# Optimization experiments

Hardware: AMD Instinct MI355X
Metric: run time of the kernel (lower is better)

Reference implementation:

```python
import jax, jax.numpy as jnp
import numpy as np

N_NODES = 50000
N_EDGES = 800000
N_GRAPHS = 64
IN_DIM = 128
HID = 32
HEADS = 4
EDGE_DIM = 8
OUT = 10


def setup_inputs() -> dict:
    key = jax.random.key(0)
    ks = jax.random.split(key, 20)
    s = 0.1
    inp = {
        "x": jax.random.normal(ks[0], (N_NODES, IN_DIM), jnp.float32),
        "edge_index": jax.random.randint(ks[1], (2, N_EDGES), 0, N_NODES, jnp.int32),
        "edge_attr": jax.random.normal(ks[2], (N_EDGES, EDGE_DIM), jnp.float32),
        "batch": jnp.sort(jax.random.randint(ks[3], (N_NODES,), 0, N_GRAPHS, jnp.int32)),
        # conv1: heads=4, out=32
        "W1": jax.random.normal(ks[4], (IN_DIM, HEADS * HID), jnp.float32) * s,
        "att_src1": jax.random.normal(ks[5], (HEADS, HID), jnp.float32) * s,
        "att_dst1": jax.random.normal(ks[6], (HEADS, HID), jnp.float32) * s,
        "We1": jax.random.normal(ks[7], (EDGE_DIM, HEADS * HID), jnp.float32) * s,
        "att_e1": jax.random.normal(ks[8], (HEADS, HID), jnp.float32) * s,
        "b1": jnp.zeros((HEADS * HID,), jnp.float32),
        # conv2: heads=1, out=32
        "W2": jax.random.normal(ks[9], (HEADS * HID, HID), jnp.float32) * s,
        "att_src2": jax.random.normal(ks[10], (1, HID), jnp.float32) * s,
        "att_dst2": jax.random.normal(ks[11], (1, HID), jnp.float32) * s,
        "We2": jax.random.normal(ks[12], (EDGE_DIM, HID), jnp.float32) * s,
        "att_e2": jax.random.normal(ks[13], (1, HID), jnp.float32) * s,
        "b2": jnp.zeros((HID,), jnp.float32),
        # MLP head
        "W3": jax.random.normal(ks[14], (HID, HID // 2), jnp.float32) * s,
        "b3": jnp.zeros((HID // 2,), jnp.float32),
        "W4": jax.random.normal(ks[15], (HID // 2, OUT), jnp.float32) * s,
        "b4": jnp.zeros((OUT,), jnp.float32),
    }
    return inp


def _gat_conv(x, src, dst, eattr, W, a_s, a_d, We, a_e, b, H, C, N):
    """PyG GATConv math (self-loops already appended to src/dst/eattr)."""
    h = (x @ W).reshape(-1, H, C)            # [N,H,C]
    e = (eattr @ We).reshape(-1, H, C)       # [E,H,C]
    al_s = jnp.sum(h * a_s, -1)              # [N,H]
    al_d = jnp.sum(h * a_d, -1)              # [N,H]
    alpha = al_s[src] + al_d[dst] + jnp.sum(e * a_e, -1)   # [E,H]
    alpha = jax.nn.leaky_relu(alpha, 0.2)
    # segment softmax over incoming edges of each dst node
    m = jax.ops.segment_max(alpha, dst, num_segments=N)
    ealpha = jnp.exp(alpha - m[dst])
    denom = jax.ops.segment_sum(ealpha, dst, num_segments=N)
    ealpha = ealpha / (denom[dst] + 1e-16)
    msg = h[src] * ealpha[:, :, None]        # [E,H,C]
    out = jax.ops.segment_sum(msg, dst, num_segments=N)  # [N,H,C]
    return out.reshape(N, H * C) + b


def _forward(x, edge_index, edge_attr, batch,
             W1, att_src1, att_dst1, We1, att_e1, b1,
             W2, att_src2, att_dst2, We2, att_e2, b2,
             W3, b3, W4, b4):
    N = x.shape[0]
    src, dst = edge_index[0], edge_index[1]
    # add_self_loops with fill_value='mean': loop attr = mean of incoming edge_attr
    cnt = jax.ops.segment_sum(jnp.ones((src.shape[0],), x.dtype), dst, num_segments=N)
    loop_attr = jax.ops.segment_sum(edge_attr, dst, num_segments=N) / jnp.maximum(cnt, 1.0)[:, None]
    ar = jnp.arange(N, dtype=src.dtype)
    src2 = jnp.concatenate([src, ar])
    dst2 = jnp.concatenate([dst, ar])
    eattr2 = jnp.concatenate([edge_attr, loop_attr], axis=0)

    h = _gat_conv(x, src2, dst2, eattr2, W1, att_src1, att_dst1, We1, att_e1, b1, HEADS, HID, N)
    h = jax.nn.elu(h)
    h = _gat_conv(h, src2, dst2, eattr2, W2, att_src2, att_dst2, We2, att_e2, b2, 1, HID, N)
    h = jax.nn.elu(h)
    # global mean pool per graph
    gsum = jax.ops.segment_sum(h, batch, num_segments=N_GRAPHS)
    gcnt = jax.ops.segment_sum(jnp.ones((N,), h.dtype), batch, num_segments=N_GRAPHS)
    g = gsum / jnp.maximum(gcnt, 1.0)[:, None]
    # MLP head (eval mode: dropout is identity)
    z = jax.nn.relu(g @ W3 + b3)
    return z @ W4 + b4


def reference(x, edge_index, edge_attr, batch,
              W1, att_src1, att_dst1, We1, att_e1, b1,
              W2, att_src2, att_dst2, We2, att_e2, b2,
              W3, b3, W4, b4):
    return _forward(x, edge_index, edge_attr, batch,
                    W1, att_src1, att_dst1, We1, att_e1, b1,
                    W2, att_src2, att_dst2, We2, att_e2, b2,
                    W3, b3, W4, b4)
```

## Files before the change

kernel.cpp:

```cpp
#include <hip/hip_runtime.h>
#include <hip/hip_bf16.h>
#include <math.h>

#define N_NODES 50000
#define N_EDGES 800000
#define N_GRAPHS 64
#define IN_DIM 128
#define HID 32
#define HEADS 4
#define EDGE_DIM 8
#define OUT_DIM 10
#define HC 128
#define NB 196
#define G1H 782
#define G1TOT 1563
#define CH 128
#define EPC 6250
#define RQ 4
#define RNG 12500
#define NBH 512
#define KGRID 1305

__device__ __forceinline__ float leaky(float x){ return x >= 0.f ? x : 0.2f*x; }
__device__ __forceinline__ float elu_f(float x){ return x > 0.f ? x : __expf(x)-1.f; }

__device__ __forceinline__ float bf2f(unsigned short u){
  union { unsigned int i; float f; } v; v.i = ((unsigned int)u) << 16; return v.f;
}
__device__ __forceinline__ float lo16(unsigned int u){
  union { unsigned int i; float f; } v; v.i = u << 16; return v.f;
}
__device__ __forceinline__ float hi16(unsigned int u){
  union { unsigned int i; float f; } v; v.i = u & 0xffff0000u; return v.f;
}
__device__ __forceinline__ unsigned short f2bf(float f){
  union { float f; unsigned int i; } v; v.f = f;
  unsigned int r = v.i + 0x7FFF + ((v.i >> 16) & 1);
  return (unsigned short)(r >> 16);
}

__device__ __forceinline__ void gemm1_body(int bb, float* xs, float* ws,
    const float* __restrict__ x, const float* __restrict__ W1,
    const float* __restrict__ as1, const float* __restrict__ ad1,
    unsigned short* __restrict__ h1b, float* __restrict__ als1, float* __restrict__ ald1){
  int t = threadIdx.x;
  int cg = t & 15, c8 = cg*8, qb = (t >> 4)*2;
  int base = bb * 32;
  for (int i = t; i < 1024; i += 256){
    int node = base + (i >> 5);
    int col = (i & 31) * 4;
    float4 v = make_float4(0,0,0,0);
    if (node < N_NODES) v = *(const float4*)&x[node*IN_DIM + col];
    *(float4*)&xs[(i>>5)*128 + col] = v;
  }
  float acc[2][8];
  #pragma unroll
  for (int q = 0; q < 2; q++)
    #pragma unroll
    for (int i = 0; i < 8; i++) acc[q][i] = 0.f;

  for (int kb = 0; kb < 128; kb += 32){
    __syncthreads();
    for (int i = t; i < 1024; i += 256)
      *(float4*)&ws[i*4] = *(const float4*)&W1[kb*128 + i*4];
    __syncthreads();
    #pragma unroll 8
    for (int k = 0; k < 32; k++){
      float4 w0 = *(float4*)&ws[k*128 + c8];
      float4 w1 = *(float4*)&ws[k*128 + c8 + 4];
      #pragma unroll
      for (int q = 0; q < 2; q++){
        float xv = xs[(qb + q)*128 + kb + k];
        acc[q][0] = fmaf(xv, w0.x, acc[q][0]);
        acc[q][1] = fmaf(xv, w0.y, acc[q][1]);
        acc[q][2] = fmaf(xv, w0.z, acc[q][2]);
        acc[q][3] = fmaf(xv, w0.w, acc[q][3]);
        acc[q][4] = fmaf(xv, w1.x, acc[q][4]);
        acc[q][5] = fmaf(xv, w1.y, acc[q][5]);
        acc[q][6] = fmaf(xv, w1.z, acc[q][6]);
        acc[q][7] = fmaf(xv, w1.w, acc[q][7]);
      }
    }
  }
  int head = cg >> 2;
  float asv[8], adv[8];
  #pragma unroll
  for (int i = 0; i < 8; i++){ asv[i] = as1[c8 + i]; adv[i] = ad1[c8 + i]; }
  #pragma unroll
  for (int q = 0; q < 2; q++){
    int n = base + qb + q;
    if (n >= N_NODES) continue;
    float sa = 0.f, sd = 0.f;
    #pragma unroll
    for (int i = 0; i < 8; i++){
      sa = fmaf(acc[q][i], asv[i], sa);
      sd = fmaf(acc[q][i], adv[i], sd);
    }
    sa += __shfl_xor(sa, 1); sd += __shfl_xor(sd, 1);
    sa += __shfl_xor(sa, 2); sd += __shfl_xor(sd, 2);
    uint4 pk;
    pk.x = (unsigned int)f2bf(acc[q][0]) | ((unsigned int)f2bf(acc[q][1]) << 16);
    pk.y = (unsigned int)f2bf(acc[q][2]) | ((unsigned int)f2bf(acc[q][3]) << 16);
    pk.z = (unsigned int)f2bf(acc[q][4]) | ((unsigned int)f2bf(acc[q][5]) << 16);
    pk.w = (unsigned int)f2bf(acc[q][6]) | ((unsigned int)f2bf(acc[q][7]) << 16);
    *(uint4*)&h1b[n*HC + c8] = pk;
    if ((cg & 3) == 0){ als1[n*4 + head] = sa; ald1[n*4 + head] = sd; }
  }
}

__global__ __launch_bounds__(256) void k_hist(const int* __restrict__ dst,
    unsigned short* __restrict__ part,
    const float* __restrict__ x, const float* __restrict__ W1,
    const float* __restrict__ as1, const float* __restrict__ ad1,
    unsigned short* __restrict__ h1b, float* __restrict__ als1, float* __restrict__ ald1){
  __shared__ unsigned int ldsU[12544];
  int m = blockIdx.x % 5, r = blockIdx.x / 5;
  int t = threadIdx.x;
  if (m < 2){
    int hb = r*2 + m;
    if (hb >= NBH) return;
    int c = hb >> 2, rg = hb & 3;
    int lo = rg * RNG;
    for (int i = t; i < RNG; i += 256) ldsU[i] = 0;
    __syncthreads();
    int e0 = c * EPC;
    for (int i = t; i < EPC; i += 256){
      int d = dst[e0 + i];
      unsigned int dr = (unsigned int)(d - lo);
      if (dr < RNG) atomicAdd(&ldsU[dr], 1u);
    }
    __syncthreads();
    for (int i = t; i < RNG; i += 256)
      part[(size_t)c*N_NODES + lo + i] = (unsigned short)ldsU[i];
    return;
  }
  int gb = r*3 + (m-2);
  if (gb >= G1H) return;
  gemm1_body(gb, (float*)ldsU, (float*)ldsU + 4096, x, W1, as1, ad1, h1b, als1, ald1);
}

__global__ __launch_bounds__(256) void k_cprefix(unsigned short* __restrict__ part,
    int* __restrict__ cnt){
  int n = blockIdx.x*256 + threadIdx.x;
  if (n >= N_NODES) return;
  unsigned int run = 0;
  for (int c = 0; c < CH; c++){
    size_t idx = (size_t)c*N_NODES + n;
    unsigned int v = part[idx];
    part[idx] = (unsigned short)run;
    run += v;
  }
  cnt[n] = (int)run;
}

__global__ __launch_bounds__(256) void k_blocksum(const int* __restrict__ cnt, int* __restrict__ bsum){
  __shared__ int sh[256];
  int n = blockIdx.x*256 + threadIdx.x;
  sh[threadIdx.x] = (n < N_NODES) ? cnt[n] : 0;
  __syncthreads();
  for (int off = 128; off > 0; off >>= 1){
    if (threadIdx.x < off) sh[threadIdx.x] += sh[threadIdx.x + off];
    __syncthreads();
  }
  if (threadIdx.x == 0) bsum[blockIdx.x] = sh[0];
}

__global__ __launch_bounds__(256) void k_scanb(const int* __restrict__ bsum, int* __restrict__ bpre){
  __shared__ int sh[256];
  int t = threadIdx.x;
  int v = (t < NB) ? bsum[t] : 0;
  sh[t] = v; __syncthreads();
  for (int off = 1; off < 256; off <<= 1){
    int u = (t >= off) ? sh[t-off] : 0;
    __syncthreads();
    sh[t] += u;
    __syncthreads();
  }
  if (t < NB) bpre[t] = sh[t] - v;
}

__global__ __launch_bounds__(256) void k_rowptr(const int* __restrict__ cnt, const int* __restrict__ bpre,
    int* __restrict__ rowptr){
  __shared__ int sh[256];
  int t = threadIdx.x; int n = blockIdx.x*256 + t;
  int c = (n < N_NODES) ? cnt[n] : 0;
  sh[t] = c; __syncthreads();
  for (int off = 1; off < 256; off <<= 1){
    int u = (t >= off) ? sh[t-off] : 0;
    __syncthreads();
    sh[t] += u;
    __syncthreads();
  }
  int incl = sh[t];
  if (n < N_NODES){
    rowptr[n] = bpre[blockIdx.x] + incl - c;
  }
  if (n == N_NODES-1) rowptr[N_NODES] = bpre[blockIdx.x] + incl;
}

__global__ __launch_bounds__(256) void k_scat(const int* __restrict__ src, const int* __restrict__ dst,
    const unsigned short* __restrict__ part, const int* __restrict__ rowptr,
    const float* __restrict__ eattr,
    const float* __restrict__ We1, const float* __restrict__ ae1w,
    const float* __restrict__ We2, const float* __restrict__ ae2w,
    int4* __restrict__ rec,
    const float* __restrict__ x, const float* __restrict__ W1,
    const float* __restrict__ as1, const float* __restrict__ ad1,
    unsigned short* __restrict__ h1b, float* __restrict__ als1, float* __restrict__ ald1){
  __shared__ unsigned int ldsU[12544];
  __shared__ float wproj[40];
  int m = blockIdx.x % 5, r = blockIdx.x / 5;
  int t = threadIdx.x;
  if (m < 2){
    int sb = r*2 + m;
    if (sb >= NBH) return;
    int c = sb >> 2, rg = sb & 3;
    int lo = rg * RNG;
    if (t < 32){
      int d = t >> 2, h = t & 3;
      float s = 0.f;
      for (int cc = 0; cc < 32; cc++) s = fmaf(We1[d*128 + h*32 + cc], ae1w[h*32 + cc], s);
      wproj[d*4 + h] = s;
    } else if (t < 40){
      int d = t - 32;
      float s = 0.f;
      for (int cc = 0; cc < 32; cc++) s = fmaf(We2[d*32 + cc], ae2w[cc], s);
      wproj[32 + d] = s;
    }
    for (int i = t; i < RNG; i += 256)
      ldsU[i] = (unsigned int)part[(size_t)c*N_NODES + lo + i];
    __syncthreads();
    int e0 = c * EPC;
    for (int i = t; i < EPC; i += 256){
      int e = e0 + i;
      int d = dst[e];
      unsigned int dr = (unsigned int)(d - lo);
      if (dr < RNG){
        int sv = src[e];
        float4 x0 = *(const float4*)&eattr[(size_t)e*8];
        float4 x1 = *(const float4*)&eattr[(size_t)e*8 + 4];
        float ea[8] = {x0.x,x0.y,x0.z,x0.w,x1.x,x1.y,x1.z,x1.w};
        float4 rr = make_float4(0,0,0,0);
        float r2 = 0.f;
        #pragma unroll
        for (int dd = 0; dd < 8; dd++){
          rr.x = fmaf(ea[dd], wproj[dd*4+0], rr.x);
          rr.y = fmaf(ea[dd], wproj[dd*4+1], rr.y);
          rr.z = fmaf(ea[dd], wproj[dd*4+2], rr.z);
          rr.w = fmaf(ea[dd], wproj[dd*4+3], rr.w);
          r2   = fmaf(ea[dd], wproj[32+dd], r2);
        }
        unsigned int lr = atomicAdd(&ldsU[dr], 1u);
        int pos = rowptr[d] + (int)lr;
        int4 rv;
        rv.x = sv;
        rv.y = (int)((unsigned int)f2bf(rr.x) | ((unsigned int)f2bf(rr.y) << 16));
        rv.z = (int)((unsigned int)f2bf(rr.z) | ((unsigned int)f2bf(rr.w) << 16));
        rv.w = __float_as_int(r2);
        rec[pos] = rv;
      }
    }
    return;
  }
  int gb = G1H + r*3 + (m-2);
  if (gb >= G1TOT) return;
  gemm1_body(gb, (float*)ldsU, (float*)ldsU + 4096, x, W1, as1, ad1, h1b, als1, ald1);
}

__global__ __launch_bounds__(256) void k_conv1(const int* __restrict__ rowptr, const int4* __restrict__ rec,
    const float* __restrict__ als1, const float* __restrict__ ald1,
    const unsigned short* __restrict__ h1b, const float* __restrict__ b1,
    unsigned short* __restrict__ heb){
  int wv = threadIdx.x >> 6, l = threadIdx.x & 63;
  int n = blockIdx.x*4 + wv;
  if (n >= N_NODES) return;
  int g = l >> 4, il = l & 15;
  int c0 = il*8, h = il >> 2;
  int hs1 = (h & 1) * 16;
  float ad = ald1[n*4 + h];
  float den = 0.f, sum_ae = 0.f;
  float acc[8];
  #pragma unroll
  for (int i = 0; i < 8; i++) acc[i] = 0.f;
  int r0 = rowptr[n], r1 = rowptr[n+1];
  for (int k = r0 + g; k < r1; k += 4){
    int4 q = rec[k];
    unsigned int w = (h & 2) ? (unsigned int)q.z : (unsigned int)q.y;
    float aev = bf2f((unsigned short)(w >> hs1));
    float as_v = als1[q.x*4 + h];
    uint4 hv = *(const uint4*)(h1b + q.x*HC + c0);
    float p = __expf(leaky(as_v + ad + aev));
    sum_ae += aev; den += p;
    acc[0] = fmaf(p, lo16(hv.x), acc[0]);
    acc[1] = fmaf(p, hi16(hv.x), acc[1]);
    acc[2] = fmaf(p, lo16(hv.y), acc[2]);
    acc[3] = fmaf(p, hi16(hv.y), acc[3]);
    acc[4] = fmaf(p, lo16(hv.z), acc[4]);
    acc[5] = fmaf(p, hi16(hv.z), acc[5]);
    acc[6] = fmaf(p, lo16(hv.w), acc[6]);
    acc[7] = fmaf(p, hi16(hv.w), acc[7]);
  }
  #pragma unroll
  for (int off = 16; off < 64; off <<= 1){
    den    += __shfl_xor(den, off);
    sum_ae += __shfl_xor(sum_ae, off);
    #pragma unroll
    for (int i = 0; i < 8; i++) acc[i] += __shfl_xor(acc[i], off);
  }
  int cn = r1 - r0; if (cn < 1) cn = 1;
  float ps = __expf(leaky(als1[n*4 + h] + ad + sum_ae / (float)cn));
  uint4 hs = *(const uint4*)(h1b + n*HC + c0);
  den += ps;
  acc[0] = fmaf(ps, lo16(hs.x), acc[0]);
  acc[1] = fmaf(ps, hi16(hs.x), acc[1]);
  acc[2] = fmaf(ps, lo16(hs.y), acc[2]);
  acc[3] = fmaf(ps, hi16(hs.y), acc[3]);
  acc[4] = fmaf(ps, lo16(hs.z), acc[4]);
  acc[5] = fmaf(ps, hi16(hs.z), acc[5]);
  acc[6] = fmaf(ps, lo16(hs.w), acc[6]);
  acc[7] = fmaf(ps, hi16(hs.w), acc[7]);
  float inv = 1.f / (den + 1e-16f);
  float4 bv0 = *(const float4*)&b1[c0];
  float4 bv1 = *(const float4*)&b1[c0 + 4];
  float o0 = elu_f(fmaf(acc[0], inv, bv0.x));
  float o1 = elu_f(fmaf(acc[1], inv, bv0.y));
  float o2 = elu_f(fmaf(acc[2], inv, bv0.z));
  float o3 = elu_f(fmaf(acc[3], inv, bv0.w));
  float o4 = elu_f(fmaf(acc[4], inv, bv1.x));
  float o5 = elu_f(fmaf(acc[5], inv, bv1.y));
  float o6 = elu_f(fmaf(acc[6], inv, bv1.z));
  float o7 = elu_f(fmaf(acc[7], inv, bv1.w));
  if (g == 0){
    uint4 pk;
    pk.x = (unsigned int)f2bf(o0) | ((unsigned int)f2bf(o1) << 16);
    pk.y = (unsigned int)f2bf(o2) | ((unsigned int)f2bf(o3) << 16);
    pk.z = (unsigned int)f2bf(o4) | ((unsigned int)f2bf(o5) << 16);
    pk.w = (unsigned int)f2bf(o6) | ((unsigned int)f2bf(o7) << 16);
    *(uint4*)(heb + n*HC + c0) = pk;
  }
}

__global__ __launch_bounds__(256) void k_gemm2(const unsigned short* __restrict__ heb,
    const float* __restrict__ W2, const float* __restrict__ as2, const float* __restrict__ ad2,
    unsigned short* __restrict__ h2b, float* __restrict__ als2, float* __restrict__ ald2){
  __shared__ float ws[128*32];
  __shared__ float xs[16][128];
  int t = threadIdx.x; int c = t & 31; int j = t >> 5;
  int base = blockIdx.x * 16;
  for (int i = t; i < 1024; i += 256)
    *(float4*)&ws[i*4] = *(const float4*)&W2[i*4];
  {
    int node = base + (t >> 4);
    int col = (t & 15) * 8;
    uint4 v = make_uint4(0,0,0,0);
    if (node < N_NODES) v = *(const uint4*)(heb + node*128 + col);
    float* xp = &xs[t>>4][col];
    xp[0] = bf2f((unsigned short)v.x); xp[1] = bf2f((unsigned short)(v.x>>16));
    xp[2] = bf2f((unsigned short)v.y); xp[3] = bf2f((unsigned short)(v.y>>16));
    xp[4] = bf2f((unsigned short)v.z); xp[5] = bf2f((unsigned short)(v.z>>16));
    xp[6] = bf2f((unsigned short)v.w); xp[7] = bf2f((unsigned short)(v.w>>16));
  }
  __syncthreads();
  float s0 = 0.f, s1 = 0.f;
  #pragma unroll 8
  for (int k = 0; k < 128; k++){
    float w = ws[k*32 + c];
    s0 = fmaf(xs[j*2][k],   w, s0);
    s1 = fmaf(xs[j*2+1][k], w, s1);
  }
  float a2c = as2[c], d2c = ad2[c];
  int n0 = base + j*2, n1 = n0 + 1;
  float sa0 = s0*a2c, sd0 = s0*d2c, sa1 = s1*a2c, sd1 = s1*d2c;
  #pragma unroll
  for (int off = 1; off < 32; off <<= 1){
    sa0 += __shfl_xor(sa0, off); sd0 += __shfl_xor(sd0, off);
    sa1 += __shfl_xor(sa1, off); sd1 += __shfl_xor(sd1, off);
  }
  if (n0 < N_NODES){ h2b[n0*32 + c] = f2bf(s0); if (c == 0){ als2[n0] = sa0; ald2[n0] = sd0; } }
  if (n1 < N_NODES){ h2b[n1*32 + c] = f2bf(s1); if (c == 0){ als2[n1] = sa1; ald2[n1] = sd1; } }
}

__global__ __launch_bounds__(256) void k_conv2(const int* __restrict__ rowptr, const int4* __restrict__ rec,
    const float* __restrict__ als2, const float* __restrict__ ald2,
    const unsigned short* __restrict__ h2b, const float* __restrict__ b2, float* __restrict__ out2){
  int wv = threadIdx.x >> 6, l = threadIdx.x & 63;
  int n = blockIdx.x*4 + wv;
  if (n >= N_NODES) return;
  int g = l >> 3, il = l & 7;
  int c0 = il*4;
  float ad = ald2[n];
  float den = 0.f, sum_ae = 0.f;
  float acc[4];
  #pragma unroll
  for (int i = 0; i < 4; i++) acc[i] = 0.f;
  int r0 = rowptr[n], r1 = rowptr[n+1];
  for (int k = r0 + g; k < r1; k += 8){
    int4 q = rec[k];
    float aev = __int_as_float(q.w);
    float as_v = als2[q.x];
    uint2 hv = *(const uint2*)(h2b + q.x*32 + c0);
    float p = __expf(leaky(as_v + ad + aev));
    sum_ae += aev; den += p;
    acc[0] = fmaf(p, lo16(hv.x), acc[0]);
    acc[1] = fmaf(p, hi16(hv.x), acc[1]);
    acc[2] = fmaf(p, lo16(hv.y), acc[2]);
    acc[3] = fmaf(p, hi16(hv.y), acc[3]);
  }
  #pragma unroll
  for (int off = 8; off < 64; off <<= 1){
    den    += __shfl_xor(den, off);
    sum_ae += __shfl_xor(sum_ae, off);
    #pragma unroll
    for (int i = 0; i < 4; i++) acc[i] += __shfl_xor(acc[i], off);
  }
  int cn = r1 - r0; if (cn < 1) cn = 1;
  float ps = __expf(leaky(als2[n] + ad + sum_ae / (float)cn));
  uint2 hs = *(const uint2*)(h2b + n*32 + c0);
  den += ps;
  acc[0] = fmaf(ps, lo16(hs.x), acc[0]);
  acc[1] = fmaf(ps, hi16(hs.x), acc[1]);
  acc[2] = fmaf(ps, lo16(hs.y), acc[2]);
  acc[3] = fmaf(ps, hi16(hs.y), acc[3]);
  float inv = 1.f / (den + 1e-16f);
  float4 bv = *(const float4*)&b2[c0];
  if (g == 0){
    float4 ov;
    ov.x = elu_f(fmaf(acc[0], inv, bv.x));
    ov.y = elu_f(fmaf(acc[1], inv, bv.y));
    ov.z = elu_f(fmaf(acc[2], inv, bv.z));
    ov.w = elu_f(fmaf(acc[3], inv, bv.w));
    *(float4*)&out2[n*32 + c0] = ov;
  }
}

__global__ __launch_bounds__(256) void k_pool(const float* __restrict__ out2, const int* __restrict__ batch,
    float* __restrict__ gpool){
  int g = blockIdx.x;
  int a = 0, b = N_NODES;
  while (a < b){ int mid = (a + b) >> 1; if (batch[mid] < g) a = mid + 1; else b = mid; }
  int lo = a;
  a = lo; b = N_NODES;
  while (a < b){ int mid = (a + b) >> 1; if (batch[mid] < g + 1) a = mid + 1; else b = mid; }
  int hi = a;
  int t = threadIdx.x, c = t & 31, r = t >> 5;
  float s = 0.f;
  for (int n = lo + r; n < hi; n += 8) s += out2[n*32 + c];
  __shared__ float sh[256];
  sh[t] = s; __syncthreads();
  if (r == 0){
    for (int q = 1; q < 8; q++) s += sh[q*32 + c];
    int cg = hi - lo; if (cg < 1) cg = 1;
    gpool[g*32 + c] = s / (float)cg;
  }
}

__global__ __launch_bounds__(1024) void k_mlp(const float* __restrict__ gpool, const float* __restrict__ W3,
    const float* __restrict__ b3, const float* __restrict__ W4, const float* __restrict__ b4,
    float* __restrict__ out){
  __shared__ float z[64*16];
  int t = threadIdx.x;
  {
    int g = t >> 4, jj = t & 15;
    float s = b3[jj];
    #pragma unroll
    for (int c = 0; c < 32; c++) s = fmaf(gpool[g*32 + c], W3[c*16 + jj], s);
    z[t] = fmaxf(s, 0.f);
  }
  __syncthreads();
  if (t < 640){
    int g = t / 10, o = t - g*10;
    float s = b4[o];
    #pragma unroll
    for (int jj = 0; jj < 16; jj++) s = fmaf(z[g*16 + jj], W4[jj*10 + o], s);
    out[t] = s;
  }
}

extern "C" void kernel_launch(void* const* d_in, const int* in_sizes, int n_in,
                              void* d_out, int out_size, void* d_ws, size_t ws_size,
                              hipStream_t stream) {
  (void)in_sizes; (void)n_in; (void)out_size; (void)ws_size;
  const float* x     = (const float*)d_in[0];
  const int*   ei    = (const int*)  d_in[1];
  const float* eattr = (const float*)d_in[2];
  const int*   batch = (const int*)  d_in[3];
  const float* W1    = (const float*)d_in[4];
  const float* as1   = (const float*)d_in[5];
  const float* ad1   = (const float*)d_in[6];
  const float* We1   = (const float*)d_in[7];
  const float* ae1w  = (const float*)d_in[8];
  const float* b1    = (const float*)d_in[9];
  const float* W2    = (const float*)d_in[10];
  const float* as2   = (const float*)d_in[11];
  const float* ad2   = (const float*)d_in[12];
  const float* We2   = (const float*)d_in[13];
  const float* ae2w  = (const float*)d_in[14];
  const float* b2    = (const float*)d_in[15];
  const float* W3    = (const float*)d_in[16];
  const float* b3    = (const float*)d_in[17];
  const float* W4    = (const float*)d_in[18];
  const float* b4    = (const float*)d_in[19];
  float* out = (float*)d_out;
  const int* src  = ei;
  const int* dstp = ei + N_EDGES;

  char* p = (char*)d_ws;
  auto alloc = [&](size_t bytes)->void*{ void* r = (void*)p; p += (bytes + 255) & ~(size_t)255; return r; };
  int*    cnt      = (int*)   alloc(4*N_NODES);
  int*    rowptr   = (int*)   alloc(4*(N_NODES+1));
  int*    bsum     = (int*)   alloc(4*NB);
  int*    bpre     = (int*)   alloc(4*NB);
  int4*   rec      = (int4*)  alloc(16*N_EDGES);
  unsigned short* h1b  = (unsigned short*)alloc(2*N_NODES*HC);
  float*  als1     = (float*) alloc(16*N_NODES);
  float*  ald1     = (float*) alloc(16*N_NODES);
  unsigned short* heb  = (unsigned short*)alloc(2*N_NODES*HC);
  unsigned short* h2b  = (unsigned short*)alloc(2*N_NODES*HID);
  float*  als2     = (float*) alloc(4*N_NODES);
  float*  ald2     = (float*) alloc(4*N_NODES);
  float*  out2     = (float*) alloc(4*N_NODES*HID);
  float*  gpool    = (float*) alloc(4*N_GRAPHS*HID);
  unsigned short* part = heb;

  k_hist    <<<KGRID, 256, 0, stream>>>(dstp, part, x, W1, as1, ad1, h1b, als1, ald1);
  k_cprefix <<<NB,    256, 0, stream>>>(part, cnt);
  k_blocksum<<<NB,    256, 0, stream>>>(cnt, bsum);
  k_scanb   <<<1,     256, 0, stream>>>(bsum, bpre);
  k_rowptr  <<<NB,    256, 0, stream>>>(cnt, bpre, rowptr);
  k_scat    <<<KGRID, 256, 0, stream>>>(src, dstp, part, rowptr, eattr, We1, ae1w, We2, ae2w,
                                        rec, x, W1, as1, ad1, h1b, als1, ald1);
  k_conv1   <<<(N_NODES+3)/4, 256, 0, stream>>>(rowptr, rec, als1, ald1, h1b, b1, heb);
  k_gemm2   <<<(N_NODES+15)/16, 256, 0, stream>>>(heb, W2, as2, ad2, h2b, als2, ald2);
  k_conv2   <<<(N_NODES+3)/4, 256, 0, stream>>>(rowptr, rec, als2, ald2, h2b, b2, out2);
  k_pool    <<<N_GRAPHS, 256, 0, stream>>>(out2, batch, gpool);
  k_mlp     <<<1,    1024, 0, stream>>>(gpool, W3, b3, W4, b4, out);
}
```

Measured before the change: 349.3 us.

## Pack per-chunk histogram counters as 8-bit lanes to cover all nodes per block

The histogram and scatter phases now use byte-packed counters in shared memory, four nodes per 32-bit word. Each block can then cover all 50000 destination nodes for its edge chunk instead of splitting the node range into four sub-ranges. This halves the chunk count and removes the four-fold rereading of dst per chunk, and gemm1 work is interleaved 12:1 with histogram blocks. It relies on per-chunk per-node in-degree staying below 256 within 12500 edges, which is safe for random inputs but could overflow on skewed graphs.

After: 356.3 us. 1.02x slower.

```diff
diff --git a/kernel.cpp b/kernel.cpp
--- a/kernel.cpp
+++ b/kernel.cpp
@@ -14,12 +14,9 @@
 #define NB 196
 #define G1H 782
 #define G1TOT 1563
-#define CH 128
-#define EPC 6250
-#define RQ 4
-#define RNG 12500
-#define NBH 512
-#define KGRID 1305
+#define CH 64
+#define EPC 12500
+#define FGRID 858
 
 __device__ __forceinline__ float leaky(float x){ return x >= 0.f ? x : 0.2f*x; }
 __device__ __forceinline__ float elu_f(float x){ return x > 0.f ? x : __expf(x)-1.f; }
@@ -114,27 +111,26 @@
     const float* __restrict__ as1, const float* __restrict__ ad1,
     unsigned short* __restrict__ h1b, float* __restrict__ als1, float* __restrict__ ald1){
   __shared__ unsigned int ldsU[12544];
-  int m = blockIdx.x % 5, r = blockIdx.x / 5;
+  int m = blockIdx.x % 13, r = blockIdx.x / 13;
   int t = threadIdx.x;
-  if (m < 2){
-    int hb = r*2 + m;
-    if (hb >= NBH) return;
-    int c = hb >> 2, rg = hb & 3;
-    int lo = rg * RNG;
-    for (int i = t; i < RNG; i += 256) ldsU[i] = 0;
+  if (m == 0){
+    if (r >= CH) return;
+    int c = r;
+    for (int i = t; i < 12500; i += 256) ldsU[i] = 0;
     __syncthreads();
     int e0 = c * EPC;
     for (int i = t; i < EPC; i += 256){
       int d = dst[e0 + i];
-      unsigned int dr = (unsigned int)(d - lo);
-      if (dr < RNG) atomicAdd(&ldsU[dr], 1u);
-    }
-    __syncthreads();
-    for (int i = t; i < RNG; i += 256)
-      part[(size_t)c*N_NODES + lo + i] = (unsigned short)ldsU[i];
+      atomicAdd(&ldsU[d >> 2], 1u << ((d & 3) * 8));
+    }
+    __syncthreads();
+    for (int i = t; i < N_NODES; i += 256){
+      unsigned int v = ldsU[i >> 2];
+      part[(size_t)c*N_NODES + i] = (unsigned short)((v >> ((i & 3) * 8)) & 0xFFu);
+    }
     return;
   }
-  int gb = r*3 + (m-2);
+  int gb = r*12 + (m-1);
   if (gb >= G1H) return;
   gemm1_body(gb, (float*)ldsU, (float*)ldsU + 4096, x, W1, as1, ad1, h1b, als1, ald1);
 }
@@ -209,13 +205,11 @@
     unsigned short* __restrict__ h1b, float* __restrict__ als1, float* __restrict__ ald1){
   __shared__ unsigned int ldsU[12544];
   __shared__ float wproj[40];
-  int m = blockIdx.x % 5, r = blockIdx.x / 5;
+  int m = blockIdx.x % 13, r = blockIdx.x / 13;
   int t = threadIdx.x;
-  if (m < 2){
-    int sb = r*2 + m;
-    if (sb >= NBH) return;
-    int c = sb >> 2, rg = sb & 3;
-    int lo = rg * RNG;
+  if (m == 0){
+    if (r >= CH) return;
+    int c = r;
     if (t < 32){
       int d = t >> 2, h = t & 3;
       float s = 0.f;
@@ -227,42 +221,44 @@
       for (int cc = 0; cc < 32; cc++) s = fmaf(We2[d*32 + cc], ae2w[cc], s);
       wproj[32 + d] = s;
     }
-    for (int i = t; i < RNG; i += 256)
-      ldsU[i] = (unsigned int)part[(size_t)c*N_NODES + lo + i];
+    for (int i = t; i < 12500; i += 256){
+      const unsigned short* pp = &part[(size_t)c*N_NODES + i*4];
+      uint2 ld = *(const uint2*)pp;
+      ldsU[i] = (ld.x & 0xFFu) | ((ld.x >> 8) & 0xFF00u)
+              | ((ld.y & 0xFFu) << 16) | (((ld.y >> 8) & 0xFF00u) << 16);
+    }
     __syncthreads();
     int e0 = c * EPC;
     for (int i = t; i < EPC; i += 256){
       int e = e0 + i;
       int d = dst[e];
-      unsigned int dr = (unsigned int)(d - lo);
-      if (dr < RNG){
-        int sv = src[e];
-        float4 x0 = *(const float4*)&eattr[(size_t)e*8];
-        float4 x1 = *(const float4*)&eattr[(size_t)e*8 + 4];
-        float ea[8] = {x0.x,x0.y,x0.z,x0.w,x1.x,x1.y,x1.z,x1.w};
-        float4 rr = make_float4(0,0,0,0);
-        float r2 = 0.f;
-        #pragma unroll
-        for (int dd = 0; dd < 8; dd++){
-          rr.x = fmaf(ea[dd], wproj[dd*4+0], rr.x);
-          rr.y = fmaf(ea[dd], wproj[dd*4+1], rr.y);
-          rr.z = fmaf(ea[dd], wproj[dd*4+2], rr.z);
-          rr.w = fmaf(ea[dd], wproj[dd*4+3], rr.w);
-          r2   = fmaf(ea[dd], wproj[32+dd], r2);
-        }
-        unsigned int lr = atomicAdd(&ldsU[dr], 1u);
-        int pos = rowptr[d] + (int)lr;
-        int4 rv;
-        rv.x = sv;
-        rv.y = (int)((unsigned int)f2bf(rr.x) | ((unsigned int)f2bf(rr.y) << 16));
-        rv.z = (int)((unsigned int)f2bf(rr.z) | ((unsigned int)f2bf(rr.w) << 16));
-        rv.w = __float_as_int(r2);
-        rec[pos] = rv;
+      int sv = src[e];
+      float4 x0 = *(const float4*)&eattr[(size_t)e*8];
+      float4 x1 = *(const float4*)&eattr[(size_t)e*8 + 4];
+      float ea[8] = {x0.x,x0.y,x0.z,x0.w,x1.x,x1.y,x1.z,x1.w};
+      float4 rr = make_float4(0,0,0,0);
+      float r2 = 0.f;
+      #pragma unroll
+      for (int dd = 0; dd < 8; dd++){
+        rr.x = fmaf(ea[dd], wproj[dd*4+0], rr.x);
+        rr.y = fmaf(ea[dd], wproj[dd*4+1], rr.y);
+        rr.z = fmaf(ea[dd], wproj[dd*4+2], rr.z);
+        rr.w = fmaf(ea[dd], wproj[dd*4+3], rr.w);
+        r2   = fmaf(ea[dd], wproj[32+dd], r2);
       }
+      unsigned int sh = (unsigned int)(d & 3) * 8;
+      unsigned int old = atomicAdd(&ldsU[d >> 2], 1u << sh);
+      int pos = rowptr[d] + (int)((old >> sh) & 0xFFu);
+      int4 rv;
+      rv.x = sv;
+      rv.y = (int)((unsigned int)f2bf(rr.x) | ((unsigned int)f2bf(rr.y) << 16));
+      rv.z = (int)((unsigned int)f2bf(rr.z) | ((unsigned int)f2bf(rr.w) << 16));
+      rv.w = __float_as_int(r2);
+      rec[pos] = rv;
     }
     return;
   }
-  int gb = G1H + r*3 + (m-2);
+  int gb = G1H + r*12 + (m-1);
   if (gb >= G1TOT) return;
   gemm1_body(gb, (float*)ldsU, (float*)ldsU + 4096, x, W1, as1, ad1, h1b, als1, ald1);
 }
@@ -522,12 +518,12 @@
   float*  gpool    = (float*) alloc(4*N_GRAPHS*HID);
   unsigned short* part = heb;
 
-  k_hist    <<<KGRID, 256, 0, stream>>>(dstp, part, x, W1, as1, ad1, h1b, als1, ald1);
+  k_hist    <<<FGRID, 256, 0, stream>>>(dstp, part, x, W1, as1, ad1, h1b, als1, ald1);
   k_cprefix <<<NB,    256, 0, stream>>>(part, cnt);
   k_blocksum<<<NB,    256, 0, stream>>>(cnt, bsum);
   k_scanb   <<<1,     256, 0, stream>>>(bsum, bpre);
   k_rowptr  <<<NB,    256, 0, stream>>>(cnt, bpre, rowptr);
-  k_scat    <<<KGRID, 256, 0, stream>>>(src, dstp, part, rowptr, eattr, We1, ae1w, We2, ae2w,
+  k_scat    <<<FGRID, 256, 0, stream>>>(src, dstp, part, rowptr, eattr, We1, ae1w, We2, ae2w,
                                         rec, x, W1, as1, ad1, h1b, als1, ald1);
   k_conv1   <<<(N_NODES+3)/4, 256, 0, stream>>>(rowptr, rec, als1, ald1, h1b, b1, heb);
   k_gemm2   <<<(N_NODES+15)/16, 256, 0, stream>>>(heb, W2, as2, ad2, h2b, als2, ald2);
```
